# Performance work log

Measured on AMD Instinct MI355X. Metric: run time of the kernel, lower is better.

Reference implementation:

```python
import jax, jax.numpy as jnp
import numpy as np

D = 1024  # d = D_in // 3
GAMMA = 5.0
EPS_NORM = 1e-5
EPS_W = 1e-8


def batch_affine_norm(x, g, b):
    # normalize over batch+time dims, per-feature affine
    mean = x.mean(axis=(0, 1))
    var = x.var(axis=(0, 1))
    return (x - mean) / jnp.sqrt(var + EPS_NORM) * g + b


def block(xi, w, b, a, g, beta):
    # xi: (B,T,d) -> (B,T,d,3)
    # PositiveLinearHK(1->3): softplus-positive weight + bias, per channel
    h = xi[..., None] * jax.nn.softplus(w) + b          # (B,T,d,3)
    # SingleStiefelProjector(3): orthogonalize learned 3x3 via QR, apply
    Q, _ = jnp.linalg.qr(a)                             # (d,3,3)
    h = jnp.einsum('btdi,dij->btdj', h, Q)
    return batch_affine_norm(h, g, beta)


def setup_inputs() -> dict:
    key = jax.random.key(0)
    ks = jax.random.split(key, 20)
    B, T = 4, 2048
    inp = {'x': jax.random.normal(ks[0], (B, T, 3 * D), dtype=jnp.float32)}
    i = 1
    for p in ('q', 'k', 'v'):
        inp['w' + p] = jax.random.normal(ks[i], (D, 3), dtype=jnp.float32) * 0.5; i += 1
        inp['b' + p] = jnp.zeros((D, 3), dtype=jnp.float32)
        inp['a' + p] = jax.random.normal(ks[i], (D, 3, 3), dtype=jnp.float32); i += 1
        inp['g' + p] = jnp.ones((D, 3), dtype=jnp.float32)
        inp['beta' + p] = jnp.zeros((D, 3), dtype=jnp.float32)
    inp['g_out'] = jnp.ones((D,), dtype=jnp.float32)
    inp['b_out'] = jnp.zeros((D,), dtype=jnp.float32)
    return inp


def reference(x, wq, bq, aq, gq, betaq, wk, bk, ak, gk, betak, wv, bv, av, gv, betav, g_out, b_out):
    d = D
    Qp = block(x[..., :d], wq, bq, aq, gq, betaq)        # (B,T,d,3)
    Kp = block(x[..., d:2 * d], wk, bk, ak, gk, betak)
    Vp = block(x[..., 2 * d:], wv, bv, av, gv, betav)
    scores = jax.nn.sigmoid(GAMMA * (Qp * Kp))
    weights = scores / (scores.sum(axis=-1, keepdims=True) + EPS_W)
    out = (weights * Vp).sum(axis=-1)                    # (B,T,d)
    return batch_affine_norm(out, g_out, b_out)
```

## Files before the change

### kernel.cpp

```cpp
#include <hip/hip_runtime.h>
#include <math.h>

namespace {

constexpr int DD = 1024;
constexpr int NC = 3072;
constexpr int NG = 768;
constexpr int DG = 256;
constexpr int NROWS = 8192;
constexpr float GAMMA = 5.0f;
constexpr float EPS_NORM = 1e-5f;
constexpr float EPS_W = 1e-8f;
constexpr float ZCLAMP = 15.0f;

typedef float nfloat4 __attribute__((ext_vector_type(4)));

struct Params {
  const float *x;
  const float *wq, *aq, *gq, *betaq;
  const float *wk, *ak, *gk, *betak;
  const float *wv, *av, *gv, *betav;
  const float *g_out, *b_out;
  float *out;
  float *colsum, *colsq;
  float *A_arr, *B_arr;
  float *osum, *osq;
  float *o_arr;
};

__device__ __forceinline__ void acc4(float4& s, float4& q, float4 v) {
  s.x += v.x; s.y += v.y; s.z += v.z; s.w += v.w;
  q.x += v.x * v.x; q.y += v.y * v.y; q.z += v.z * v.z; q.w += v.w * v.w;
}

__device__ __forceinline__ void qr_coef(const Params& P, int c, float mean, float var) {
  int p = c >> 10;
  int d = c & (DD - 1);
  const float* w    = (p == 0) ? P.wq    : (p == 1) ? P.wk    : P.wv;
  const float* a    = (p == 0) ? P.aq    : (p == 1) ? P.ak    : P.av;
  const float* g    = (p == 0) ? P.gq    : (p == 1) ? P.gk    : P.gv;
  const float* beta = (p == 0) ? P.betaq : (p == 1) ? P.betak : P.betav;
  float gam = (p == 0) ? GAMMA : 1.0f;

  float A[3][3];
  #pragma unroll
  for (int i = 0; i < 3; ++i)
    #pragma unroll
    for (int j = 0; j < 3; ++j) A[i][j] = a[(d * 3 + i) * 3 + j];

  float v1y = 0.f, v1z = 0.f, v2z = 0.f, t1 = 0.f, t2 = 0.f;
  {
    float alpha = A[0][0];
    float xn2 = A[1][0] * A[1][0] + A[2][0] * A[2][0];
    if (xn2 > 0.f) {
      float beta_ = -copysignf(sqrtf(alpha * alpha + xn2), alpha);
      t1 = (beta_ - alpha) / beta_;
      float inv = 1.0f / (alpha - beta_);
      v1y = A[1][0] * inv; v1z = A[2][0] * inv;
      #pragma unroll
      for (int j = 1; j < 3; ++j) {
        float dot = A[0][j] + A[1][j] * v1y + A[2][j] * v1z;
        float f = t1 * dot;
        A[0][j] -= f; A[1][j] -= f * v1y; A[2][j] -= f * v1z;
      }
    }
  }
  {
    float alpha = A[1][1], x2 = A[2][1];
    if (x2 != 0.f) {
      float beta_ = -copysignf(sqrtf(alpha * alpha + x2 * x2), alpha);
      t2 = (beta_ - alpha) / beta_;
      v2z = x2 / (alpha - beta_);
    }
  }
  float v1[3] = {1.f, v1y, v1z};
  float v2[3] = {0.f, 1.f, v2z};
  float v12 = v1y + v1z * v2z;
  float sp0 = log1pf(expf(w[d * 3 + 0]));
  float sp1 = log1pf(expf(w[d * 3 + 1]));
  float sp2 = log1pf(expf(w[d * 3 + 2]));
  #pragma unroll
  for (int j = 0; j < 3; ++j) {
    float Q0 = ((0 == j) ? 1.f : 0.f) - t1 * v1[0] * v1[j] - t2 * v2[0] * v2[j]
               + t1 * t2 * v12 * v1[0] * v2[j];
    float Q1 = ((1 == j) ? 1.f : 0.f) - t1 * v1[1] * v1[j] - t2 * v2[1] * v2[j]
               + t1 * t2 * v12 * v1[1] * v2[j];
    float Q2 = ((2 == j) ? 1.f : 0.f) - t1 * v1[2] * v1[j] - t2 * v2[2] * v2[j]
               + t1 * t2 * v12 * v1[2] * v2[j];
    float W = sp0 * Q0 + sp1 * Q1 + sp2 * Q2;
    float s = W * g[d * 3 + j] / sqrtf(W * W * var + EPS_NORM);
    P.A_arr[j * NC + c] = gam * s;
    P.B_arr[j * NC + c] = gam * (beta[d * 3 + j] - mean * s);
  }
}

struct CoefReg {
  float4 Aq[3], Bq[3], Ak[3], Bk[3], Av[3], Bv[3];
};

__device__ __forceinline__ CoefReg load_coefs(const Params& P, int tg) {
  CoefReg C;
  #pragma unroll
  for (int j = 0; j < 3; ++j) {
    C.Aq[j] = ((const float4*)(P.A_arr + j * NC))[tg];
    C.Ak[j] = ((const float4*)(P.A_arr + j * NC + DD))[tg];
    C.Av[j] = ((const float4*)(P.A_arr + j * NC + 2 * DD))[tg];
    C.Bq[j] = ((const float4*)(P.B_arr + j * NC))[tg];
    C.Bk[j] = ((const float4*)(P.B_arr + j * NC + DD))[tg];
    C.Bv[j] = ((const float4*)(P.B_arr + j * NC + 2 * DD))[tg];
  }
  return C;
}

__device__ __forceinline__ float4 contract4(float4 xq, float4 xk, float4 xv,
                                            const CoefReg& C) {
  float4 ov;
  #pragma unroll
  for (int kk = 0; kk < 4; ++kk) {
    float xqv = ((const float*)&xq)[kk];
    float xkv = ((const float*)&xk)[kk];
    float xvv = ((const float*)&xv)[kk];
    float Q[3], K[3], V[3];
    #pragma unroll
    for (int j = 0; j < 3; ++j) {
      Q[j] = fmaf(xqv, ((const float*)&C.Aq[j])[kk], ((const float*)&C.Bq[j])[kk]);
      K[j] = fmaf(xkv, ((const float*)&C.Ak[j])[kk], ((const float*)&C.Bk[j])[kk]);
      V[j] = fmaf(xvv, ((const float*)&C.Av[j])[kk], ((const float*)&C.Bv[j])[kk]);
    }
    float e0 = __expf(fminf(Q[0] * K[0], ZCLAMP));
    float e1 = __expf(fminf(Q[1] * K[1], ZCLAMP));
    float e2 = __expf(fminf(Q[2] * K[2], ZCLAMP));
    float a0 = 1.f + e0, a1 = 1.f + e1, a2 = 1.f + e2;
    float a01 = a0 * a1, a12 = a1 * a2, a02 = a0 * a2;
    float w0 = e0 * a12, w1 = e1 * a02, w2 = e2 * a01;
    float num = w0 * V[0] + w1 * V[1] + w2 * V[2];
    float den = w0 + w1 + w2 + EPS_W * (a01 * a2);
    ((float*)&ov)[kk] = num / den;
  }
  return ov;
}

__global__ __launch_bounds__(256, 4) void k1_col_stats(Params P) {
  __shared__ float4 lds_s[4][64];
  __shared__ float4 lds_q[4][64];
  const int t = threadIdx.x;
  const int lane = t & 63;
  const int slice = t >> 6;
  const int cg = blockIdx.x * 64 + lane;
  const int r0 = blockIdx.y * 128 + slice * 32;
  const float4* x4 = (const float4*)P.x;
  float4 s = {0,0,0,0}, q = {0,0,0,0};
  #pragma unroll 8
  for (int r = 0; r < 32; ++r) {
    acc4(s, q, x4[(size_t)(r0 + r) * NG + cg]);
  }
  lds_s[slice][lane] = s;
  lds_q[slice][lane] = q;
  __syncthreads();
  float ssum = 0.f, ssq = 0.f;
  #pragma unroll
  for (int i = 0; i < 4; ++i) {
    ssum += ((const float*)&lds_s[i][t >> 2])[t & 3];
    ssq  += ((const float*)&lds_q[i][t >> 2])[t & 3];
  }
  atomicAdd(&P.colsum[blockIdx.x * 256 + t], ssum);
  atomicAdd(&P.colsq[blockIdx.x * 256 + t], ssq);
}

__global__ __launch_bounds__(256, 4) void k2_coef(Params P) {
  const int c = blockIdx.x * 256 + threadIdx.x;
  float s = P.colsum[c];
  float q = P.colsq[c];
  float mean = s / NROWS;
  float var = q / NROWS - mean * mean;
  if (var < 0.f) var = 0.f;
  qr_coef(P, c, mean, var);
}

__global__ __launch_bounds__(256, 3) void k3_main(Params P) {
  __shared__ float4 lds_s[4][64];
  __shared__ float4 lds_q[4][64];
  const int t = threadIdx.x;
  const int lane = t & 63;
  const int slice = t >> 6;
  const int tg = blockIdx.x * 64 + lane;
  const int r0 = blockIdx.y * 32 + slice * 8;
  const float4* x4 = (const float4*)P.x;
  float4* o4 = (float4*)P.o_arr;
  CoefReg C = load_coefs(P, tg);
  float4 s = {0,0,0,0}, q = {0,0,0,0};
  #pragma unroll
  for (int r = 0; r < 8; ++r) {
    size_t base = (size_t)(r0 + r) * NG;
    float4 xq = x4[base + tg];
    float4 xk = x4[base + 256 + tg];
    float4 xv = x4[base + 512 + tg];
    float4 ov = contract4(xq, xk, xv, C);
    o4[(size_t)(r0 + r) * DG + tg] = ov;
    acc4(s, q, ov);
  }
  lds_s[slice][lane] = s;
  lds_q[slice][lane] = q;
  __syncthreads();
  float ssum = 0.f, ssq = 0.f;
  #pragma unroll
  for (int i = 0; i < 4; ++i) {
    ssum += ((const float*)&lds_s[i][t >> 2])[t & 3];
    ssq  += ((const float*)&lds_q[i][t >> 2])[t & 3];
  }
  atomicAdd(&P.osum[blockIdx.x * 256 + t], ssum);
  atomicAdd(&P.osq[blockIdx.x * 256 + t], ssq);
}

__global__ __launch_bounds__(256, 8) void k4_final(Params P) {
  const int t = threadIdx.x;
  float4 s4 = ((const float4*)P.osum)[t];
  float4 q4 = ((const float4*)P.osq)[t];
  float4 g4 = ((const float4*)P.g_out)[t];
  float4 b4 = ((const float4*)P.b_out)[t];
  float4 m, sc;
  #pragma unroll
  for (int kk = 0; kk < 4; ++kk) {
    float mean = ((const float*)&s4)[kk] / NROWS;
    float var = ((const float*)&q4)[kk] / NROWS - mean * mean;
    if (var < 0.f) var = 0.f;
    ((float*)&m)[kk] = mean;
    ((float*)&sc)[kk] = ((const float*)&g4)[kk] / sqrtf(var + EPS_NORM);
  }
  const int r0 = blockIdx.x * 4;
  const float4* o4 = (const float4*)P.o_arr;
  float4* out4 = (float4*)P.out;
  #pragma unroll
  for (int rr = 0; rr < 4; ++rr) {
    size_t idx = (size_t)(r0 + rr) * DG + t;
    float4 o = o4[idx];
    nfloat4 y;
    y.x = (o.x - m.x) * sc.x + b4.x;
    y.y = (o.y - m.y) * sc.y + b4.y;
    y.z = (o.z - m.z) * sc.z + b4.z;
    y.w = (o.w - m.w) * sc.w + b4.w;
    __builtin_nontemporal_store(y, (nfloat4*)&out4[idx]);
  }
}

}

extern "C" void kernel_launch(void* const* d_in, const int* in_sizes, int n_in,
                              void* d_out, int out_size, void* d_ws, size_t ws_size,
                              hipStream_t stream) {
  Params P;
  P.x     = (const float*)d_in[0];
  P.wq    = (const float*)d_in[1];
  P.aq    = (const float*)d_in[3];
  P.gq    = (const float*)d_in[4];
  P.betaq = (const float*)d_in[5];
  P.wk    = (const float*)d_in[6];
  P.ak    = (const float*)d_in[8];
  P.gk    = (const float*)d_in[9];
  P.betak = (const float*)d_in[10];
  P.wv    = (const float*)d_in[11];
  P.av    = (const float*)d_in[13];
  P.gv    = (const float*)d_in[14];
  P.betav = (const float*)d_in[15];
  P.g_out = (const float*)d_in[16];
  P.b_out = (const float*)d_in[17];
  P.out   = (float*)d_out;

  float* ws = (float*)d_ws;
  P.colsum = ws;  ws += NC;
  P.colsq  = ws;  ws += NC;
  P.osum   = ws;  ws += DD;
  P.osq    = ws;  ws += DD;
  P.A_arr  = ws;  ws += 3 * NC;
  P.B_arr  = ws;  ws += 3 * NC;
  P.o_arr  = ws;  ws += (size_t)NROWS * DD;

  (void)hipMemsetAsync(P.colsum, 0, (2 * NC + 2 * DD) * sizeof(float), stream);
  k1_col_stats<<<dim3(12, 64), dim3(256), 0, stream>>>(P);
  k2_coef<<<dim3(12), dim3(256), 0, stream>>>(P);
  k3_main<<<dim3(4, 256), dim3(256), 0, stream>>>(P);
  k4_final<<<dim3(2048), dim3(256), 0, stream>>>(P);
}
```

Measured before the change: 64.20 us.

## Fuse coefficient computation into main kernel and store intermediate in fp16

Removes the separate coefficient kernel. Each main-kernel block now recomputes the QR-derived per-channel affine coefficients for its 256 columns and shares them through LDS, which drops one launch and the round trip through global memory. The intermediate output buffer is also stored as fp16 instead of fp32, halving the write and re-read traffic between the main and final kernels. The cost is redundant QR/softplus work in all 256 row-blocks per column group, plus fp16 rounding of the pre-normalization output, which could hurt accuracy.

```diff
diff --git a/kernel.cpp b/kernel.cpp
--- a/kernel.cpp
+++ b/kernel.cpp
@@ -1,4 +1,5 @@
 #include <hip/hip_runtime.h>
+#include <hip/hip_fp16.h>
 #include <math.h>
 
 namespace {
@@ -23,9 +24,8 @@
   const float *g_out, *b_out;
   float *out;
   float *colsum, *colsq;
-  float *A_arr, *B_arr;
   float *osum, *osq;
-  float *o_arr;
+  unsigned short *o_arr;
 };
 
 __device__ __forceinline__ void acc4(float4& s, float4& q, float4 v) {
@@ -33,7 +33,8 @@
   q.x += v.x * v.x; q.y += v.y * v.y; q.z += v.z * v.z; q.w += v.w * v.w;
 }
 
-__device__ __forceinline__ void qr_coef(const Params& P, int c, float mean, float var) {
+__device__ __forceinline__ void qr_coef_reg(const Params& P, int c, float mean,
+                                            float var, float* Aout, float* Bout) {
   int p = c >> 10;
   int d = c & (DD - 1);
   const float* w    = (p == 0) ? P.wq    : (p == 1) ? P.wk    : P.wv;
@@ -89,28 +90,14 @@
                + t1 * t2 * v12 * v1[2] * v2[j];
     float W = sp0 * Q0 + sp1 * Q1 + sp2 * Q2;
     float s = W * g[d * 3 + j] / sqrtf(W * W * var + EPS_NORM);
-    P.A_arr[j * NC + c] = gam * s;
-    P.B_arr[j * NC + c] = gam * (beta[d * 3 + j] - mean * s);
+    Aout[j] = gam * s;
+    Bout[j] = gam * (beta[d * 3 + j] - mean * s);
   }
 }
 
 struct CoefReg {
   float4 Aq[3], Bq[3], Ak[3], Bk[3], Av[3], Bv[3];
 };
-
-__device__ __forceinline__ CoefReg load_coefs(const Params& P, int tg) {
-  CoefReg C;
-  #pragma unroll
-  for (int j = 0; j < 3; ++j) {
-    C.Aq[j] = ((const float4*)(P.A_arr + j * NC))[tg];
-    C.Ak[j] = ((const float4*)(P.A_arr + j * NC + DD))[tg];
-    C.Av[j] = ((const float4*)(P.A_arr + j * NC + 2 * DD))[tg];
-    C.Bq[j] = ((const float4*)(P.B_arr + j * NC))[tg];
-    C.Bk[j] = ((const float4*)(P.B_arr + j * NC + DD))[tg];
-    C.Bv[j] = ((const float4*)(P.B_arr + j * NC + 2 * DD))[tg];
-  }
-  return C;
-}
 
 __device__ __forceinline__ float4 contract4(float4 xq, float4 xk, float4 xv,
                                             const CoefReg& C) {
@@ -167,17 +154,9 @@
   atomicAdd(&P.colsq[blockIdx.x * 256 + t], ssq);
 }
 
-__global__ __launch_bounds__(256, 4) void k2_coef(Params P) {
-  const int c = blockIdx.x * 256 + threadIdx.x;
-  float s = P.colsum[c];
-  float q = P.colsq[c];
-  float mean = s / NROWS;
-  float var = q / NROWS - mean * mean;
-  if (var < 0.f) var = 0.f;
-  qr_coef(P, c, mean, var);
-}
-
-__global__ __launch_bounds__(256, 3) void k3_main(Params P) {
+__global__ __launch_bounds__(256, 3) void k2_main(Params P) {
+  __shared__ float lds_A[3][256][3];
+  __shared__ float lds_B[3][256][3];
   __shared__ float4 lds_s[4][64];
   __shared__ float4 lds_q[4][64];
   const int t = threadIdx.x;
@@ -185,9 +164,48 @@
   const int slice = t >> 6;
   const int tg = blockIdx.x * 64 + lane;
   const int r0 = blockIdx.y * 32 + slice * 8;
+
+  {
+    const int dcol = blockIdx.x * 256 + t;
+    float s = 0.f, q = 0.f, mean, var;
+    #pragma unroll
+    for (int p = 0; p < 3; ++p) {
+      int c = p * DD + dcol;
+      s = P.colsum[c];
+      q = P.colsq[c];
+      mean = s / NROWS;
+      var = q / NROWS - mean * mean;
+      if (var < 0.f) var = 0.f;
+      float Ac[3], Bc[3];
+      qr_coef_reg(P, c, mean, var, Ac, Bc);
+      #pragma unroll
+      for (int j = 0; j < 3; ++j) {
+        lds_A[p][t][j] = Ac[j];
+        lds_B[p][t][j] = Bc[j];
+      }
+    }
+  }
+  __syncthreads();
+
+  CoefReg C;
+  {
+    const int gl = (lane << 2);
+    #pragma unroll
+    for (int j = 0; j < 3; ++j) {
+      #pragma unroll
+      for (int kk = 0; kk < 4; ++kk) {
+        ((float*)&C.Aq[j])[kk] = lds_A[0][gl + kk][j];
+        ((float*)&C.Bq[j])[kk] = lds_B[0][gl + kk][j];
+        ((float*)&C.Ak[j])[kk] = lds_A[1][gl + kk][j];
+        ((float*)&C.Bk[j])[kk] = lds_B[1][gl + kk][j];
+        ((float*)&C.Av[j])[kk] = lds_A[2][gl + kk][j];
+        ((float*)&C.Bv[j])[kk] = lds_B[2][gl + kk][j];
+      }
+    }
+  }
+
   const float4* x4 = (const float4*)P.x;
-  float4* o4 = (float4*)P.o_arr;
-  CoefReg C = load_coefs(P, tg);
+  ushort4* o4 = (ushort4*)P.o_arr;
   float4 s = {0,0,0,0}, q = {0,0,0,0};
   #pragma unroll
   for (int r = 0; r < 8; ++r) {
@@ -196,7 +214,12 @@
     float4 xk = x4[base + 256 + tg];
     float4 xv = x4[base + 512 + tg];
     float4 ov = contract4(xq, xk, xv, C);
-    o4[(size_t)(r0 + r) * DG + tg] = ov;
+    ushort4 oh;
+    oh.x = __half_as_ushort(__float2half(ov.x));
+    oh.y = __half_as_ushort(__float2half(ov.y));
+    oh.z = __half_as_ushort(__float2half(ov.z));
+    oh.w = __half_as_ushort(__float2half(ov.w));
+    o4[(size_t)(r0 + r) * DG + tg] = oh;
     acc4(s, q, ov);
   }
   lds_s[slice][lane] = s;
@@ -212,7 +235,7 @@
   atomicAdd(&P.osq[blockIdx.x * 256 + t], ssq);
 }
 
-__global__ __launch_bounds__(256, 8) void k4_final(Params P) {
+__global__ __launch_bounds__(256, 8) void k3_final(Params P) {
   const int t = threadIdx.x;
   float4 s4 = ((const float4*)P.osum)[t];
   float4 q4 = ((const float4*)P.osq)[t];
@@ -228,17 +251,17 @@
     ((float*)&sc)[kk] = ((const float*)&g4)[kk] / sqrtf(var + EPS_NORM);
   }
   const int r0 = blockIdx.x * 4;
-  const float4* o4 = (const float4*)P.o_arr;
+  const ushort4* o4 = (const ushort4*)P.o_arr;
   float4* out4 = (float4*)P.out;
   #pragma unroll
   for (int rr = 0; rr < 4; ++rr) {
     size_t idx = (size_t)(r0 + rr) * DG + t;
-    float4 o = o4[idx];
+    ushort4 oh = o4[idx];
     nfloat4 y;
-    y.x = (o.x - m.x) * sc.x + b4.x;
-    y.y = (o.y - m.y) * sc.y + b4.y;
-    y.z = (o.z - m.z) * sc.z + b4.z;
-    y.w = (o.w - m.w) * sc.w + b4.w;
+    y.x = (__half2float(__ushort_as_half(oh.x)) - m.x) * sc.x + b4.x;
+    y.y = (__half2float(__ushort_as_half(oh.y)) - m.y) * sc.y + b4.y;
+    y.z = (__half2float(__ushort_as_half(oh.z)) - m.z) * sc.z + b4.z;
+    y.w = (__half2float(__ushort_as_half(oh.w)) - m.w) * sc.w + b4.w;
     __builtin_nontemporal_store(y, (nfloat4*)&out4[idx]);
   }
 }
@@ -271,13 +294,10 @@
   P.colsq  = ws;  ws += NC;
   P.osum   = ws;  ws += DD;
   P.osq    = ws;  ws += DD;
-  P.A_arr  = ws;  ws += 3 * NC;
-  P.B_arr  = ws;  ws += 3 * NC;
-  P.o_arr  = ws;  ws += (size_t)NROWS * DD;
+  P.o_arr  = (unsigned short*)ws;
 
   (void)hipMemsetAsync(P.colsum, 0, (2 * NC + 2 * DD) * sizeof(float), stream);
   k1_col_stats<<<dim3(12, 64), dim3(256), 0, stream>>>(P);
-  k2_coef<<<dim3(12), dim3(256), 0, stream>>>(P);
-  k3_main<<<dim3(4, 256), dim3(256), 0, stream>>>(P);
-  k4_final<<<dim3(2048), dim3(256), 0, stream>>>(P);
-}
+  k2_main<<<dim3(4, 256), dim3(256), 0, stream>>>(P);
+  k3_final<<<dim3(2048), dim3(256), 0, stream>>>(P);
+}
```

New measurement: 65.11 us. About the same (+1.4%).
